# Optimization experiments

Hardware: AMD Instinct MI355X
Metric: run time of the kernel (lower is better)

The kernel has to match this reference:

```python
import jax, jax.numpy as jnp
import numpy as np
from jax import lax

NUM_CLASSES = 80
IOU_THR = 0.5
SCORE_THR = 0.5
MAX_BOXES = 100
NEG = jnp.float32(-1e9)


def setup_inputs() -> dict:
    key = jax.random.key(0)
    ks = jax.random.split(key, 9)
    B = 64
    d = {}
    d['bbox13'] = jax.random.uniform(ks[0], (B, 13, 13, 3, 4), dtype=jnp.float32)
    d['p13'] = jax.random.uniform(ks[1], (B, 13, 13, 3, 1), dtype=jnp.float32)
    d['c13'] = jax.random.uniform(ks[2], (B, 13, 13, 3, NUM_CLASSES), dtype=jnp.float32)
    d['bbox26'] = jax.random.uniform(ks[3], (B, 26, 26, 3, 4), dtype=jnp.float32)
    d['p26'] = jax.random.uniform(ks[4], (B, 26, 26, 3, 1), dtype=jnp.float32)
    d['c26'] = jax.random.uniform(ks[5], (B, 26, 26, 3, NUM_CLASSES), dtype=jnp.float32)
    d['bbox52'] = jax.random.uniform(ks[6], (B, 52, 52, 3, 4), dtype=jnp.float32)
    d['p52'] = jax.random.uniform(ks[7], (B, 52, 52, 3, 1), dtype=jnp.float32)
    d['c52'] = jax.random.uniform(ks[8], (B, 52, 52, 3, NUM_CLASSES), dtype=jnp.float32)
    return d


def _nms_single(boxes, scores):
    # boxes: [N, 4] as [y1, x1, y2, x2] (normalized internally like TF), scores: [N]
    y1 = jnp.minimum(boxes[:, 0], boxes[:, 2])
    y2 = jnp.maximum(boxes[:, 0], boxes[:, 2])
    x1 = jnp.minimum(boxes[:, 1], boxes[:, 3])
    x2 = jnp.maximum(boxes[:, 1], boxes[:, 3])
    area = (y2 - y1) * (x2 - x1)
    s0 = jnp.where(scores > SCORE_THR, scores, NEG)

    def step(s, _):
        i = jnp.argmax(s)
        sc = s[i]
        valid = sc > SCORE_THR
        iy1 = jnp.maximum(y1, y1[i]); iy2 = jnp.minimum(y2, y2[i])
        ix1 = jnp.maximum(x1, x1[i]); ix2 = jnp.minimum(x2, x2[i])
        inter = jnp.maximum(iy2 - iy1, 0.0) * jnp.maximum(ix2 - ix1, 0.0)
        union = area + area[i] - inter
        iou = jnp.where(union > 0, inter / union, 0.0)
        s = jnp.where(iou > IOU_THR, NEG, s).at[i].set(NEG)
        return s, (i, sc, valid)

    _, (idx, sel_s, valid) = lax.scan(step, s0, None, length=MAX_BOXES)
    b = jnp.clip(boxes[idx], 0.0, 1.0)          # TF combined NMS: clip_boxes=True
    b = jnp.where(valid[:, None], b, 0.0)       # pad invalid with zeros
    sel_s = jnp.where(valid, sel_s, 0.0)
    cls = jnp.zeros_like(sel_s)                 # single score class -> class id 0
    return b, sel_s, cls, valid.sum().astype(jnp.int32)


def reference(bbox13, p13, c13, bbox26, p26, c26, bbox52, p52, c52):
    B = bbox13.shape[0]
    nc = c13.shape[-1]
    bbox = jnp.concatenate([bbox13.reshape(B, -1, 4), bbox26.reshape(B, -1, 4), bbox52.reshape(B, -1, 4)], axis=1)
    p = jnp.concatenate([p13.reshape(B, -1), p26.reshape(B, -1), p52.reshape(B, -1)], axis=1)
    c = jnp.concatenate([c13.reshape(B, -1, nc), c26.reshape(B, -1, nc), c52.reshape(B, -1, nc)], axis=1)
    cls_idx = jnp.argmax(c, axis=-1).astype(jnp.float32)  # quirky: class *index* scales objectness
    score = p * cls_idx                                     # [B, N]
    b, s, cl, valid = jax.vmap(_nms_single)(bbox, score)
    pred = jnp.concatenate([b, s[..., None], cl[..., None]], axis=-1)  # [B, MAX_BOXES, 6]
    return pred, valid
```

## Files before the change

kernel.cpp:

```cpp
#include <hip/hip_runtime.h>

#define NUM_CLASSES 80
#define N13 507
#define N26 2028
#define N52 8112
#define NANCH (N13 + N26 + N52)
#define BATCH 64
#define MAXB 100
#define NB 3720
#define BOFF 0xFC00u
#define KPT 11
#define TOPK 1024
#define LCAP 4096
#define LMASK (LCAP-1)
#define APB 64

typedef unsigned long long u64;

__global__ __launch_bounds__(256) void score_kernel(
    const float* __restrict__ c13, const float* __restrict__ p13,
    const float* __restrict__ c26, const float* __restrict__ p26,
    const float* __restrict__ c52, const float* __restrict__ p52,
    float* __restrict__ scores)
{
    int a   = blockIdx.x * APB + (threadIdx.x >> 2);
    int sub = threadIdx.x & 3;
    int b   = blockIdx.y;
    if (a >= NANCH) return;
    const float* cbase; const float* pbase;
    if (a < N13)            { cbase = c13 + ((size_t)b*N13 + a) * NUM_CLASSES;           pbase = p13 + (size_t)b*N13 + a; }
    else if (a < N13+N26)   { cbase = c26 + ((size_t)b*N26 + (a-N13)) * NUM_CLASSES;     pbase = p26 + (size_t)b*N26 + (a-N13); }
    else                    { cbase = c52 + ((size_t)b*N52 + (a-N13-N26)) * NUM_CLASSES; pbase = p52 + (size_t)b*N52 + (a-N13-N26); }
    float mx = -1.0f; int mi = 0;
    #pragma unroll
    for (int q = 0; q < 5; ++q) {
        float4 v = *(const float4*)(cbase + q*16 + sub*4);
        int cb = q*16 + sub*4;
        if (v.x > mx) { mx = v.x; mi = cb+0; }
        if (v.y > mx) { mx = v.y; mi = cb+1; }
        if (v.z > mx) { mx = v.z; mi = cb+2; }
        if (v.w > mx) { mx = v.w; mi = cb+3; }
    }
    #pragma unroll
    for (int off = 1; off < 4; off <<= 1) {
        float ov = __shfl_xor(mx, off);
        int   oi = __shfl_xor(mi, off);
        if (ov > mx || (ov == mx && oi < mi)) { mx = ov; mi = oi; }
    }
    if (sub == 0) scores[(size_t)b*NANCH + a] = pbase[0] * (float)mi;
}

__device__ __forceinline__ float4 load_box(const float* __restrict__ b13,
                                           const float* __restrict__ b26,
                                           const float* __restrict__ b52,
                                           int b, int n)
{
    if (n < N13)          return *(const float4*)(b13 + ((size_t)b*N13 + n)*4);
    else if (n < N13+N26) return *(const float4*)(b26 + ((size_t)b*N26 + (n-N13))*4);
    else                  return *(const float4*)(b52 + ((size_t)b*N52 + (n-N13-N26))*4);
}

__global__ __launch_bounds__(1024) void nms_sort_scan(
    const float* __restrict__ scores,
    const float* __restrict__ b13, const float* __restrict__ b26, const float* __restrict__ b52,
    float* __restrict__ out)
{
    const int b    = blockIdx.x;
    const int tid  = threadIdx.x;
    const int lane = tid & 63;
    const int wid  = tid >> 6;

    __shared__ u64 lst[LCAP];
    __shared__ unsigned int cnt[NB];
    __shared__ unsigned int wtot[16];
    __shared__ float4 acc4[MAXB];
    __shared__ float4 cbb[64];
    __shared__ u64 sup_lds[16];
    __shared__ float outrec[MAXB][6];
    __shared__ int accN_s, T_s, L_s;

    const float* sc = scores + (size_t)b * NANCH;

    float sreg[KPT];
    #pragma unroll
    for (int k = 0; k < KPT; ++k) {
        int n = tid + (k << 10);
        sreg[k] = (n < NANCH) ? sc[n] : 0.f;
    }

    for (int i = tid; i < NB; i += 1024) cnt[i] = 0u;
    if (tid == 0) accN_s = 0;
    __syncthreads();

    #pragma unroll
    for (int k = 0; k < KPT; ++k) {
        float s = sreg[k];
        if (s > 0.5f) {
            unsigned int bk = (__float_as_uint(s) >> 14) - BOFF;
            if (bk >= NB) bk = NB - 1;
            atomicAdd(&cnt[bk], 1u);
        }
    }
    __syncthreads();

    unsigned int loc[4]; unsigned int s4 = 0u;
    #pragma unroll
    for (int q = 0; q < 4; ++q) {
        int r = tid*4 + q;
        unsigned int v = (r < NB) ? cnt[NB-1-r] : 0u;
        loc[q] = v; s4 += v;
    }
    unsigned int incl = s4;
    #pragma unroll
    for (int off = 1; off < 64; off <<= 1) {
        unsigned int v = __shfl_up(incl, off);
        if (lane >= off) incl += v;
    }
    if (lane == 63) wtot[wid] = incl;
    __syncthreads();
    unsigned int wexcl = 0u, total = 0u;
    #pragma unroll
    for (int w = 0; w < 16; ++w) { unsigned int t = wtot[w]; if (w < wid) wexcl += t; total += t; }
    unsigned int run = wexcl + (incl - s4);
    if (tid == 0) { T_s = 0; L_s = (int)total; }
    __syncthreads();
    #pragma unroll
    for (int q = 0; q < 4; ++q) {
        int r = tid*4 + q;
        if (r < NB) {
            int bk = NB-1-r;
            unsigned int c = loc[q];
            if (run < TOPK && run + c >= TOPK) { T_s = bk; L_s = (int)(run + c); }
            cnt[bk] = run;
            run += c;
        }
    }
    __syncthreads();
    const int total_i = (int)total;
    int Treg = T_s;
    int regionEnd = L_s;

    #pragma unroll
    for (int k = 0; k < KPT; ++k) {
        float s = sreg[k];
        if (s > 0.5f) {
            unsigned int bits = __float_as_uint(s);
            unsigned int bk = (bits >> 14) - BOFF;
            if (bk >= NB) bk = NB - 1;
            if ((int)bk >= Treg) {
                unsigned int pos = atomicAdd(&cnt[bk], 1u);
                lst[pos & LMASK] = ((u64)bits << 32) | (u64)(0xFFFFFFFFu - (unsigned int)(tid + (k<<10)));
            }
        }
    }
    __syncthreads();

    {
        u64 kk[4]; int tt[4];
        #pragma unroll
        for (int i = 0; i < 4; ++i) {
            int p = tid + (i << 10);
            tt[i] = -1; kk[i] = 0ull;
            if (p < regionEnd) {
                u64 key = lst[p & LMASK];
                unsigned int bk = (unsigned int)(key >> 46) - BOFF;
                if (bk >= NB) bk = NB - 1;
                unsigned int st = (bk+1 < NB) ? cnt[bk+1] : 0u;
                unsigned int e  = cnt[bk];
                unsigned int rank = 0u;
                for (unsigned int q = st; q < e; ++q) rank += (lst[q & LMASK] > key) ? 1u : 0u;
                kk[i] = key; tt[i] = (int)(st + rank);
            }
        }
        __syncthreads();
        #pragma unroll
        for (int i = 0; i < 4; ++i) if (tt[i] >= 0) lst[tt[i] & LMASK] = kk[i];
        __syncthreads();
    }

    int accN = 0;
    u64 key = 0ull; float4 bb = make_float4(0.f,0.f,0.f,0.f); float s = 0.f;
    if (lane < regionEnd) {
        key = lst[lane];
        unsigned int n = 0xFFFFFFFFu - (unsigned int)(key & 0xFFFFFFFFull);
        s = __uint_as_float((unsigned int)(key >> 32));
        bb = load_box(b13, b26, b52, b, (int)n);
    }

    int c = 0;
    while (c < total_i && accN < MAXB) {
        while (c + 64 > regionEnd && regionEnd < total_i) {
            int K2 = regionEnd + TOPK;
            if (tid == 0) { T_s = 0; L_s = total_i; }
            __syncthreads();
            for (int bk = tid; bk < Treg; bk += 1024) {
                unsigned int stv = cnt[bk];
                unsigned int ev  = (bk == 0) ? (unsigned int)total_i : cnt[bk-1];
                if (stv < (unsigned int)K2 && ev >= (unsigned int)K2) { T_s = bk; L_s = (int)ev; }
            }
            __syncthreads();
            int T2 = T_s, L2 = L_s;
            #pragma unroll
            for (int k = 0; k < KPT; ++k) {
                float sv = sreg[k];
                if (sv > 0.5f) {
                    unsigned int bits = __float_as_uint(sv);
                    int bk = (int)((bits >> 14) - BOFF);
                    if (bk >= NB) bk = NB - 1;
                    if (bk >= T2 && bk < Treg) {
                        unsigned int pos = atomicAdd(&cnt[bk], 1u);
                        lst[pos & LMASK] = ((u64)bits << 32) | (u64)(0xFFFFFFFFu - (unsigned int)(tid + (k<<10)));
                    }
                }
            }
            __syncthreads();
            {
                u64 kk[4]; int tt[4];
                #pragma unroll
                for (int i = 0; i < 4; ++i) {
                    int p = regionEnd + tid + (i << 10);
                    tt[i] = -1; kk[i] = 0ull;
                    if (p < L2) {
                        u64 k2 = lst[p & LMASK];
                        unsigned int bk = (unsigned int)(k2 >> 46) - BOFF;
                        if (bk >= NB) bk = NB - 1;
                        unsigned int st = (bk+1 < NB) ? cnt[bk+1] : 0u;
                        unsigned int e  = cnt[bk];
                        unsigned int rank = 0u;
                        for (unsigned int q = st; q < e; ++q) rank += (lst[q & LMASK] > k2) ? 1u : 0u;
                        kk[i] = k2; tt[i] = (int)(st + rank);
                    }
                }
                __syncthreads();
                #pragma unroll
                for (int i = 0; i < 4; ++i) if (tt[i] >= 0) lst[tt[i] & LMASK] = kk[i];
                __syncthreads();
            }
            Treg = T2; regionEnd = L2;
            key = 0ull; bb = make_float4(0.f,0.f,0.f,0.f); s = 0.f;
            if (c + lane < regionEnd) {
                key = lst[(c + lane) & LMASK];
                unsigned int n = 0xFFFFFFFFu - (unsigned int)(key & 0xFFFFFFFFull);
                s = __uint_as_float((unsigned int)(key >> 32));
                bb = load_box(b13, b26, b52, b, (int)n);
            }
        }

        int m = regionEnd - c; if (m > 64) m = 64;
        float oy1 = bb.x, ox1 = bb.y, oy2 = bb.z, ox2 = bb.w, cs = s;
        float y1 = fminf(oy1, oy2), y2 = fmaxf(oy1, oy2);
        float x1 = fminf(ox1, ox2), x2 = fmaxf(ox1, ox2);
        float ar = (y2-y1)*(x2-x1);

        int nc = c + 64;
        if (nc + lane < regionEnd) {
            key = lst[(nc + lane) & LMASK];
            unsigned int n = 0xFFFFFFFFu - (unsigned int)(key & 0xFFFFFFFFull);
            s = __uint_as_float((unsigned int)(key >> 32));
            bb = load_box(b13, b26, b52, b, (int)n);
        } else { s = 0.f; bb = make_float4(0.f,0.f,0.f,0.f); }

        bool supp = (lane >= m);
        #pragma unroll 2
        for (int j = wid; j < accN; j += 16) {
            float4 aj = acc4[j];
            float jar = (aj.z - aj.x) * (aj.w - aj.y);
            float iy1=fmaxf(y1,aj.x), iy2=fminf(y2,aj.z);
            float ix1=fmaxf(x1,aj.y), ix2=fminf(x2,aj.w);
            float inter=fmaxf(iy2-iy1,0.f)*fmaxf(ix2-ix1,0.f);
            float un=(ar+jar)-inter;
            supp |= (un > 0.f) && (inter/un > 0.5f);
        }
        u64 bal = __ballot(supp);
        if (lane == 0) sup_lds[wid] = bal;

        u64 myrow = 0ull;
        if (wid == 0) {
            cbb[lane] = make_float4(y1, x1, y2, x2);
            #pragma unroll 4
            for (int k = 0; k < m; ++k) {
                float4 ck = cbb[k];
                float kar = (ck.z - ck.x) * (ck.w - ck.y);
                float iy1=fmaxf(y1,ck.x), iy2=fminf(y2,ck.z);
                float ix1=fmaxf(x1,ck.y), ix2=fminf(x2,ck.w);
                float inter=fmaxf(iy2-iy1,0.f)*fmaxf(ix2-ix1,0.f);
                float un=(ar+kar)-inter;
                if ((un > 0.f) && (inter/un > 0.5f)) myrow |= (1ull << k);
            }
        }
        __syncthreads();

        if (wid == 0) {
            u64 B = 0ull;
            #pragma unroll
            for (int w = 0; w < 16; ++w) B |= sup_lds[w];
            u64 valid_m = (m >= 64) ? ~0ull : ((1ull << m) - 1ull);
            u64 rem = (~B) & valid_m;
            u64 accmask = 0ull;
            const int start = accN;
            while (rem && accN < MAXB) {
                int j = __builtin_ctzll(rem);
                u64 rowj = (u64)(unsigned int)__builtin_amdgcn_readlane((int)(myrow & 0xFFFFFFFFull), j)
                         | ((u64)(unsigned int)__builtin_amdgcn_readlane((int)(myrow >> 32), j) << 32);
                accmask |= (1ull << j);
                rem &= ~rowj;
                rem &= ~(1ull << j);
                accN++;
            }
            if (accmask & (1ull << lane)) {
                int pos = start + (int)__popcll(accmask & ((1ull << lane) - 1ull));
                acc4[pos] = make_float4(y1, x1, y2, x2);
                outrec[pos][0]=fminf(fmaxf(oy1,0.f),1.f);
                outrec[pos][1]=fminf(fmaxf(ox1,0.f),1.f);
                outrec[pos][2]=fminf(fmaxf(oy2,0.f),1.f);
                outrec[pos][3]=fminf(fmaxf(ox2,0.f),1.f);
                outrec[pos][4]=cs;
                outrec[pos][5]=0.f;
            }
            if (lane == 0) accN_s = accN;
        }
        __syncthreads();
        accN = accN_s;
        c += 64;
    }

    const int accNf = accN_s;
    float* outp = out + (size_t)b * (MAXB*6);
    for (int i = tid; i < MAXB*6; i += 1024) {
        int t = i / 6;
        outp[i] = (t < accNf) ? outrec[t][i % 6] : 0.f;
    }
    if (tid == 0) out[(size_t)BATCH*(MAXB*6) + b] = (float)accNf;
}

extern "C" void kernel_launch(void* const* d_in, const int* in_sizes, int n_in,
                              void* d_out, int out_size, void* d_ws, size_t ws_size,
                              hipStream_t stream)
{
    const float* bbox13 = (const float*)d_in[0];
    const float* p13    = (const float*)d_in[1];
    const float* c13    = (const float*)d_in[2];
    const float* bbox26 = (const float*)d_in[3];
    const float* p26    = (const float*)d_in[4];
    const float* c26    = (const float*)d_in[5];
    const float* bbox52 = (const float*)d_in[6];
    const float* p52    = (const float*)d_in[7];
    const float* c52    = (const float*)d_in[8];
    float* out    = (float*)d_out;
    float* scores = (float*)d_ws;

    dim3 g1((NANCH + APB - 1)/APB, BATCH);
    score_kernel<<<g1, 256, 0, stream>>>(c13, p13, c26, p26, c52, p52, scores);
    nms_sort_scan<<<BATCH, 1024, 0, stream>>>(scores, bbox13, bbox26, bbox52, out);
}
```

Measured before the change: 69.95 us.

## Precompute IoU suppression bitmask matrix for first 512 candidates before chunked NMS

New measurement: 103.8 us. 1.48x slower.

```diff
diff --git a/kernel.cpp b/kernel.cpp
--- a/kernel.cpp
+++ b/kernel.cpp
@@ -14,8 +14,19 @@
 #define LCAP 4096
 #define LMASK (LCAP-1)
 #define APB 64
+#define MW 512
 
 typedef unsigned long long u64;
+
+__device__ __forceinline__ bool sup_cmp(float inter, float un) {
+    return (un > 0.f) && ((double)inter > 0x1.000001p-1 * (double)un);
+}
+
+__device__ __forceinline__ u64 readlane64(u64 v, int l) {
+    unsigned int lo = (unsigned int)__builtin_amdgcn_readlane((int)(v & 0xFFFFFFFFull), l);
+    unsigned int hi = (unsigned int)__builtin_amdgcn_readlane((int)(v >> 32), l);
+    return ((u64)hi << 32) | (u64)lo;
+}
 
 __global__ __launch_bounds__(256) void score_kernel(
     const float* __restrict__ c13, const float* __restrict__ p13,
@@ -78,6 +89,12 @@
     __shared__ u64 sup_lds[16];
     __shared__ float outrec[MAXB][6];
     __shared__ int accN_s, T_s, L_s;
+    __shared__ float4 obox[MW];
+    __shared__ float  oscor[MW];
+    __shared__ float4 cbx[MW];
+    __shared__ float  car[MW];
+    __shared__ u64    mat[8][MW + 4];
+    __shared__ u64    accword[8];
 
     const float* sc = scores + (size_t)b * NANCH;
 
@@ -178,16 +195,96 @@
         __syncthreads();
     }
 
-    int accN = 0;
+    int W = total_i; if (W > regionEnd) W = regionEnd; if (W > MW) W = MW;
+
+    if (tid < W) {
+        u64 key = lst[tid];
+        unsigned int n = 0xFFFFFFFFu - (unsigned int)(key & 0xFFFFFFFFull);
+        float4 bbv = load_box(b13, b26, b52, b, (int)n);
+        obox[tid]  = bbv;
+        oscor[tid] = __uint_as_float((unsigned int)(key >> 32));
+        float y1 = fminf(bbv.x, bbv.z), y2 = fmaxf(bbv.x, bbv.z);
+        float x1 = fminf(bbv.y, bbv.w), x2 = fmaxf(bbv.y, bbv.w);
+        cbx[tid] = make_float4(y1, x1, y2, x2);
+        car[tid] = (y2 - y1) * (x2 - x1);
+    }
+    __syncthreads();
+
+    for (int task = tid; task < 8 * MW; task += 1024) {
+        int i = task & (MW - 1), w = task >> 9;
+        if (i < W) {
+            int kbase = w << 6;
+            int kend = W - kbase; if (kend > 64) kend = 64;
+            float4 ci = cbx[i]; float iar = car[i];
+            u64 bits = 0ull;
+            for (int k = 0; k < kend; ++k) {
+                float4 cj = cbx[kbase + k];
+                float jar = car[kbase + k];
+                float iy1 = fmaxf(ci.x, cj.x), iy2 = fminf(ci.z, cj.z);
+                float ix1 = fmaxf(ci.y, cj.y), ix2 = fminf(ci.w, cj.w);
+                float inter = fmaxf(iy2 - iy1, 0.f) * fmaxf(ix2 - ix1, 0.f);
+                float un = (iar + jar) - inter;
+                if (sup_cmp(inter, un)) bits |= (1ull << k);
+            }
+            mat[w][i] = bits;
+        }
+    }
+    __syncthreads();
+
+    if (wid == 0) {
+        u64 remw = 0ull;
+        if (lane < 8) {
+            int base = lane << 6;
+            int nb = W - base;
+            remw = (nb >= 64) ? ~0ull : ((nb > 0) ? ((1ull << nb) - 1ull) : 0ull);
+        }
+        u64 accw = 0ull;
+        int acc = 0;
+        while (acc < MAXB) {
+            u64 bal = __ballot(remw != 0ull);
+            if (bal == 0ull) break;
+            int fw = (int)__builtin_ctzll(bal);
+            u64 w0 = readlane64(remw, fw);
+            int j  = (fw << 6) + (int)__builtin_ctzll(w0);
+            u64 rowl = 0ull;
+            if (lane < 8) rowl = mat[lane][j];
+            if (lane == (j >> 6)) accw |= (1ull << (j & 63));
+            if (lane < 8) remw &= ~rowl;
+            acc++;
+        }
+        if (lane < 8) accword[lane] = accw;
+        if (lane == 0) accN_s = acc;
+    }
+    __syncthreads();
+
+    int accN = accN_s;
+    if (tid < W) {
+        int w = tid >> 6, bpos = tid & 63;
+        u64 aw = accword[w];
+        if ((aw >> bpos) & 1ull) {
+            int pos = (int)__popcll(aw & ((1ull << bpos) - 1ull));
+            for (int q = 0; q < w; ++q) pos += (int)__popcll(accword[q]);
+            float4 ob = obox[tid];
+            acc4[pos] = cbx[tid];
+            outrec[pos][0] = fminf(fmaxf(ob.x, 0.f), 1.f);
+            outrec[pos][1] = fminf(fmaxf(ob.y, 0.f), 1.f);
+            outrec[pos][2] = fminf(fmaxf(ob.z, 0.f), 1.f);
+            outrec[pos][3] = fminf(fmaxf(ob.w, 0.f), 1.f);
+            outrec[pos][4] = oscor[tid];
+            outrec[pos][5] = 0.f;
+        }
+    }
+    __syncthreads();
+
     u64 key = 0ull; float4 bb = make_float4(0.f,0.f,0.f,0.f); float s = 0.f;
-    if (lane < regionEnd) {
-        key = lst[lane];
+    int c = W;
+    if (accN < MAXB && c + lane < regionEnd) {
+        key = lst[(c + lane) & LMASK];
         unsigned int n = 0xFFFFFFFFu - (unsigned int)(key & 0xFFFFFFFFull);
         s = __uint_as_float((unsigned int)(key >> 32));
         bb = load_box(b13, b26, b52, b, (int)n);
     }
 
-    int c = 0;
     while (c < total_i && accN < MAXB) {
         while (c + 64 > regionEnd && regionEnd < total_i) {
             int K2 = regionEnd + TOPK;
@@ -269,7 +366,7 @@
             float ix1=fmaxf(x1,aj.y), ix2=fminf(x2,aj.w);
             float inter=fmaxf(iy2-iy1,0.f)*fmaxf(ix2-ix1,0.f);
             float un=(ar+jar)-inter;
-            supp |= (un > 0.f) && (inter/un > 0.5f);
+            supp |= sup_cmp(inter, un);
         }
         u64 bal = __ballot(supp);
         if (lane == 0) sup_lds[wid] = bal;
@@ -285,7 +382,7 @@
                 float ix1=fmaxf(x1,ck.y), ix2=fminf(x2,ck.w);
                 float inter=fmaxf(iy2-iy1,0.f)*fmaxf(ix2-ix1,0.f);
                 float un=(ar+kar)-inter;
-                if ((un > 0.f) && (inter/un > 0.5f)) myrow |= (1ull << k);
+                if (sup_cmp(inter, un)) myrow |= (1ull << k);
             }
         }
         __syncthreads();
@@ -300,8 +397,7 @@
             const int start = accN;
             while (rem && accN < MAXB) {
                 int j = __builtin_ctzll(rem);
-                u64 rowj = (u64)(unsigned int)__builtin_amdgcn_readlane((int)(myrow & 0xFFFFFFFFull), j)
-                         | ((u64)(unsigned int)__builtin_amdgcn_readlane((int)(myrow >> 32), j) << 32);
+                u64 rowj = readlane64(myrow, j);
                 accmask |= (1ull << j);
                 rem &= ~rowj;
                 rem &= ~(1ull << j);
```
